# Optimization experiments

Hardware: AMD Instinct MI355X
Metric: run time of the kernel (lower is better)

Reference implementation:

```python
import jax, jax.numpy as jnp
import numpy as np

# AntModel forward, expressed at the ant-count level.
# Original: builds per-batch ragged routing tables where every ant at source
# neuron s is routed by the layer to a destination neuron; counts at each
# destination are accumulated, relu'd, and destinations with zero ants are
# pruned from the table (a no-op on the count vector itself). The deterministic
# layer routing used here is dest[s] = argmax(weights[s, :]).

B = 256
DIMS = [(4096, 4096), (4096, 4096), (4096, 1024)]
MAX_ANTS = 8


def setup_inputs() -> dict:
    key = jax.random.key(0)
    kx, k1, k2, k3 = jax.random.split(key, 4)
    x = jax.random.randint(kx, (B, DIMS[0][0]), 0, MAX_ANTS).astype(jnp.int32)
    W1 = jax.random.normal(k1, DIMS[0], dtype=jnp.float32)
    W2 = jax.random.normal(k2, DIMS[1], dtype=jnp.float32)
    W3 = jax.random.normal(k3, DIMS[2], dtype=jnp.float32)
    return {"x": x, "W1": W1, "W2": W2, "W3": W3}


def _layer(counts, W):
    # counts: [B, n_in] int32 ant counts; W: [n_in, n_out] pheromone weights
    dest = jnp.argmax(W, axis=1)  # [n_in] routing table
    n_out = W.shape[1]
    out = jnp.zeros((counts.shape[0], n_out), dtype=counts.dtype)
    out = out.at[:, dest].add(counts)  # scatter-add counts to destinations
    return jnp.maximum(out, 0)  # layer.relu_func (identity on counts)


def reference(x, W1, W2, W3):
    counts = x.astype(jnp.int32)
    for W in (W1, W2, W3):
        counts = _layer(counts, W)
    return counts.astype(jnp.float32)
```

## Files before the change

kernel.cpp:

```cpp
#include <hip/hip_runtime.h>


#define N_IN   4096
#define N_MID  4096
#define N_OUT  1024
#define BATCH  256

__device__ __forceinline__ void upd(float v, int idx, float& bv, int& bi) {
    if (v > bv || (v == bv && idx < bi)) { bv = v; bi = idx; }
}

template <int NCOLS>
__device__ __forceinline__ void row_argmax(const float* __restrict__ W, int row,
                                           int* __restrict__ dest) {
    const int lane = threadIdx.x & 63;
    const float4* __restrict__ p =
        reinterpret_cast<const float4*>(W + (size_t)row * NCOLS) + lane;
    constexpr int ITERS = NCOLS / 256;

    float4 v[ITERS];
    #pragma unroll
    for (int t = 0; t < ITERS; ++t)
        v[t] = p[(size_t)t * 64];
    __builtin_amdgcn_sched_barrier(0);

    float bv = -__builtin_huge_valf();
    int bi = 0;
    #pragma unroll
    for (int t = 0; t < ITERS; ++t) {
        int c = t * 256 + lane * 4;
        upd(v[t].x, c + 0, bv, bi);
        upd(v[t].y, c + 1, bv, bi);
        upd(v[t].z, c + 2, bv, bi);
        upd(v[t].w, c + 3, bv, bi);
    }
    #pragma unroll
    for (int off = 1; off < 64; off <<= 1) {
        float ov = __shfl_xor(bv, off, 64);
        int   oi = __shfl_xor(bi, off, 64);
        if (ov > bv || (ov == bv && oi < bi)) { bv = ov; bi = oi; }
    }
    if (lane == 0) dest[row] = bi;
}

__global__ __launch_bounds__(256) void argmax_all_kernel(
    const float* __restrict__ W1, const float* __restrict__ W2,
    const float* __restrict__ W3, int* __restrict__ dest1,
    int* __restrict__ dest2, int* __restrict__ dest3) {
    const int wave = (blockIdx.x * blockDim.x + threadIdx.x) >> 6;
    if (wave < N_IN) {
        row_argmax<N_MID>(W1, wave, dest1);
    } else if (wave < N_IN + N_MID) {
        row_argmax<N_MID>(W2, wave - N_IN, dest2);
    } else {
        row_argmax<N_OUT>(W3, wave - (N_IN + N_MID), dest3);
    }
}

__global__ __launch_bounds__(256) void compose_kernel(
    const int* __restrict__ dest1, const int* __restrict__ dest2,
    const int* __restrict__ dest3, int* __restrict__ fdest) {
    const int s = blockIdx.x * blockDim.x + threadIdx.x;
    if (s < N_IN) fdest[s] = dest3[dest2[dest1[s]]];
}

__global__ __launch_bounds__(1024) void scatter_kernel(
    const int* __restrict__ x, const int* __restrict__ fdest,
    float* __restrict__ out) {
    __shared__ int cnt[N_OUT];
    const int b   = blockIdx.x;
    const int tid = threadIdx.x;
    cnt[tid] = 0;
    __syncthreads();
    const int4 v = reinterpret_cast<const int4*>(x + (size_t)b * N_IN)[tid];
    const int4 d = reinterpret_cast<const int4*>(fdest)[tid];
    atomicAdd(&cnt[d.x], v.x);
    atomicAdd(&cnt[d.y], v.y);
    atomicAdd(&cnt[d.z], v.z);
    atomicAdd(&cnt[d.w], v.w);
    __syncthreads();
    out[(size_t)b * N_OUT + tid] = (float)cnt[tid];
}

extern "C" void kernel_launch(void* const* d_in, const int* in_sizes, int n_in,
                              void* d_out, int out_size, void* d_ws, size_t ws_size,
                              hipStream_t stream) {
    const int*   x  = (const int*)d_in[0];
    const float* W1 = (const float*)d_in[1];
    const float* W2 = (const float*)d_in[2];
    const float* W3 = (const float*)d_in[3];
    float* out = (float*)d_out;

    int* ws    = (int*)d_ws;
    int* dest1 = ws;
    int* dest2 = ws + N_IN;
    int* dest3 = ws + 2 * N_IN;
    int* fdest = ws + 3 * N_IN;

    const int total_waves = N_IN + N_MID + N_MID;
    argmax_all_kernel<<<total_waves / 4, 256, 0, stream>>>(W1, W2, W3,
                                                           dest1, dest2, dest3);
    compose_kernel<<<N_IN / 256, 256, 0, stream>>>(dest1, dest2, dest3, fdest);
    scatter_kernel<<<BATCH, 1024, 0, stream>>>(x, fdest, out);
}
```

Measured before the change: 172.8 us.

## Restructure argmax into 1024-thread blocks with packed-key reductions across rows

Replaces the one-wave-per-row argmax with 1024-thread blocks that each process 8 rows. Every wave reduces a 256-column chunk with a single 64-bit packed value/index key and shuffles, and an LDS stage then combines the per-wave partials. The change also fixes the total launch at 1152 blocks and prefetches the next row's float4 while reducing the current one. The aim is better memory coalescing and latency hiding for the bandwidth-bound scan of W, at the cost of more shuffle work per element and a block-wide sync.

```diff
diff --git a/kernel.cpp b/kernel.cpp
--- a/kernel.cpp
+++ b/kernel.cpp
@@ -6,54 +6,81 @@
 #define N_OUT  1024
 #define BATCH  256
 
-__device__ __forceinline__ void upd(float v, int idx, float& bv, int& bi) {
-    if (v > bv || (v == bv && idx < bi)) { bv = v; bi = idx; }
+__device__ __forceinline__ unsigned long long pack_key(float v, int idx) {
+    unsigned b = __float_as_uint(v);
+    unsigned u = (b & 0x80000000u) ? ~b : (b | 0x80000000u);
+    return ((unsigned long long)u << 32) | (unsigned)(~idx);
 }
 
-template <int NCOLS>
-__device__ __forceinline__ void row_argmax(const float* __restrict__ W, int row,
-                                           int* __restrict__ dest) {
-    const int lane = threadIdx.x & 63;
-    const float4* __restrict__ p =
-        reinterpret_cast<const float4*>(W + (size_t)row * NCOLS) + lane;
-    constexpr int ITERS = NCOLS / 256;
-
-    float4 v[ITERS];
-    #pragma unroll
-    for (int t = 0; t < ITERS; ++t)
-        v[t] = p[(size_t)t * 64];
-    __builtin_amdgcn_sched_barrier(0);
-
-    float bv = -__builtin_huge_valf();
-    int bi = 0;
-    #pragma unroll
-    for (int t = 0; t < ITERS; ++t) {
-        int c = t * 256 + lane * 4;
-        upd(v[t].x, c + 0, bv, bi);
-        upd(v[t].y, c + 1, bv, bi);
-        upd(v[t].z, c + 2, bv, bi);
-        upd(v[t].w, c + 3, bv, bi);
-    }
-    #pragma unroll
-    for (int off = 1; off < 64; off <<= 1) {
-        float ov = __shfl_xor(bv, off, 64);
-        int   oi = __shfl_xor(bi, off, 64);
-        if (ov > bv || (ov == bv && oi < bi)) { bv = ov; bi = oi; }
-    }
-    if (lane == 0) dest[row] = bi;
-}
-
-__global__ __launch_bounds__(256) void argmax_all_kernel(
+__global__ __launch_bounds__(1024, 8) void argmax_all_kernel(
     const float* __restrict__ W1, const float* __restrict__ W2,
     const float* __restrict__ W3, int* __restrict__ dest1,
     int* __restrict__ dest2, int* __restrict__ dest3) {
-    const int wave = (blockIdx.x * blockDim.x + threadIdx.x) >> 6;
-    if (wave < N_IN) {
-        row_argmax<N_MID>(W1, wave, dest1);
-    } else if (wave < N_IN + N_MID) {
-        row_argmax<N_MID>(W2, wave - N_IN, dest2);
-    } else {
-        row_argmax<N_OUT>(W3, wave - (N_IN + N_MID), dest3);
+    __shared__ unsigned long long partials[8][16];
+    const int tid  = threadIdx.x;
+    const int w    = tid >> 6;
+    const int lane = tid & 63;
+    const int blk  = blockIdx.x;
+
+    const float* Wm;
+    int kLoc;
+    if (blk < 512)       { Wm = W1; kLoc = blk; }
+    else if (blk < 1024) { Wm = W2; kLoc = blk - 512; }
+    else                 { Wm = W3; kLoc = blk - 1024; }
+    const bool isW3 = (blk >= 1024);
+
+    const float4* __restrict__ p = reinterpret_cast<const float4*>(Wm);
+    const size_t base = ((size_t)(8 * kLoc) << 10) + tid;
+    const int c = (isW3 ? (tid & 255) : tid) * 4;
+
+    float4 cur = p[base];
+    #pragma unroll
+    for (int j = 0; j < 8; ++j) {
+        float4 nxt = cur;
+        if (j < 7) nxt = p[base + ((size_t)(j + 1) << 10)];
+        __builtin_amdgcn_sched_barrier(0);
+
+        float bv = cur.x; int bi = c;
+        if (cur.y > bv) { bv = cur.y; bi = c + 1; }
+        if (cur.z > bv) { bv = cur.z; bi = c + 2; }
+        if (cur.w > bv) { bv = cur.w; bi = c + 3; }
+        unsigned long long key = pack_key(bv, bi);
+        #pragma unroll
+        for (int off = 1; off < 64; off <<= 1) {
+            unsigned long long o = __shfl_xor(key, off, 64);
+            if (o > key) key = o;
+        }
+        if (lane == 0) partials[j][w] = key;
+        cur = nxt;
+    }
+    __syncthreads();
+
+    if (tid < 128) {
+        const int j = tid >> 4, slot = tid & 15;
+        unsigned long long key = partials[j][slot];
+        if (!isW3) {
+            #pragma unroll
+            for (int off = 1; off < 16; off <<= 1) {
+                unsigned long long o = __shfl_xor(key, off, 64);
+                if (o > key) key = o;
+            }
+            if (slot == 0) {
+                int idx = (int)~(unsigned)(key & 0xFFFFFFFFull);
+                int row = 8 * kLoc + j;
+                if (blk < 512) dest1[row] = idx; else dest2[row] = idx;
+            }
+        } else {
+            #pragma unroll
+            for (int off = 1; off < 4; off <<= 1) {
+                unsigned long long o = __shfl_xor(key, off, 64);
+                if (o > key) key = o;
+            }
+            if ((slot & 3) == 0) {
+                int idx = (int)~(unsigned)(key & 0xFFFFFFFFull);
+                int g = 8 * kLoc + j;
+                dest3[4 * g + (slot >> 2)] = idx;
+            }
+        }
     }
 }
 
@@ -97,9 +124,8 @@
     int* dest3 = ws + 2 * N_IN;
     int* fdest = ws + 3 * N_IN;
 
-    const int total_waves = N_IN + N_MID + N_MID;
-    argmax_all_kernel<<<total_waves / 4, 256, 0, stream>>>(W1, W2, W3,
-                                                           dest1, dest2, dest3);
+    argmax_all_kernel<<<1152, 1024, 0, stream>>>(W1, W2, W3,
+                                                 dest1, dest2, dest3);
     compose_kernel<<<N_IN / 256, 256, 0, stream>>>(dest1, dest2, dest3, fdest);
     scatter_kernel<<<BATCH, 1024, 0, stream>>>(x, fdest, out);
 }
```

After: 173.9 us. About the same (+0.6%).
